# Performance work log

Hardware: AMD Instinct MI355X
Metric: run time of the kernel (lower is better)

The kernel has to match this reference:

```python
import jax, jax.numpy as jnp
import numpy as np

B, T = 8192, 26
V, E, H, L = 23, 100, 128, 64  # vocab, emb dim, GRU hidden, latent; LSTM hidden = E


def setup_inputs() -> dict:
    key = jax.random.key(0)
    ks = jax.random.split(key, 16)
    rn = lambda k, shape, scale=0.1: (jax.random.normal(k, shape, jnp.float32) * scale)
    emb = rn(ks[0], (V, E)).at[0].set(0.0)  # padding_idx=0 row zeroed
    return {
        "z": jax.random.normal(ks[1], (B, L), jnp.float32),
        "x_in": jax.random.randint(ks[2], (B, T), 0, V),
        "emb": emb,
        "fc_z_w": rn(ks[3], (H, L)), "fc_z_b": rn(ks[4], (H,)),
        "gru_wih": rn(ks[5], (3 * H, E)), "gru_whh": rn(ks[6], (3 * H, H)),
        "gru_bih": rn(ks[7], (3 * H,)), "gru_bhh": rn(ks[8], (3 * H,)),
        "lstm_wih": rn(ks[9], (4 * E, H)), "lstm_whh": rn(ks[10], (4 * E, E)),
        "lstm_bih": rn(ks[11], (4 * E,)), "lstm_bhh": rn(ks[12], (4 * E,)),
        "out_w": rn(ks[13], (V, E)), "out_b": rn(ks[14], (V,)),
    }


def _gru(e, h0, Wih, Whh, bih, bhh):
    # e: (B,T,E); precompute input projections for all steps, scan over T.
    xg = jnp.einsum('bti,gi->btg', e, Wih) + bih  # (B,T,3H)

    def step(h, x):
        hg = h @ Whh.T + bhh
        xr, xz, xn = jnp.split(x, 3, axis=-1)
        hr, hz, hn = jnp.split(hg, 3, axis=-1)
        r = jax.nn.sigmoid(xr + hr)
        zg = jax.nn.sigmoid(xz + hz)
        n = jnp.tanh(xn + r * hn)
        h_new = (1.0 - zg) * n + zg * h
        return h_new, h_new

    _, ys = jax.lax.scan(step, h0, jnp.swapaxes(xg, 0, 1))  # (T,B,H)
    return jnp.swapaxes(ys, 0, 1)


def _lstm(x, h0, c0, Wih, Whh, bih, bhh):
    xg = jnp.einsum('bti,gi->btg', x, Wih) + bih  # (B,T,4E)

    def step(hc, xt):
        h, c = hc
        g = xt + h @ Whh.T + bhh
        i, f, gg, o = jnp.split(g, 4, axis=-1)
        c_new = jax.nn.sigmoid(f) * c + jax.nn.sigmoid(i) * jnp.tanh(gg)
        h_new = jax.nn.sigmoid(o) * jnp.tanh(c_new)
        return (h_new, c_new), h_new

    _, ys = jax.lax.scan(step, (h0, c0), jnp.swapaxes(xg, 0, 1))
    return jnp.swapaxes(ys, 0, 1)


def reference(z, x_in, emb, fc_z_w, fc_z_b, gru_wih, gru_whh, gru_bih, gru_bhh,
              lstm_wih, lstm_whh, lstm_bih, lstm_bhh, out_w, out_b):
    h0 = jnp.tanh(z @ fc_z_w.T + fc_z_b)            # (B,H)
    e = emb[x_in]                                    # (B,T,E)
    y = _gru(e, h0, gru_wih, gru_whh, gru_bih, gru_bhh)           # (B,T,H)
    zeros = jnp.zeros((z.shape[0], E), dtype=z.dtype)
    y = _lstm(y, zeros, zeros, lstm_wih, lstm_whh, lstm_bih, lstm_bhh)  # (B,T,E)
    logits = jnp.einsum('bte,ve->btv', y, out_w) + out_b          # (B,T,V)
    return logits
```

## Files before the change

### kernel.cpp

```cpp
#include <hip/hip_runtime.h>
#include <stdint.h>
#include <stddef.h>

#define BB 8192
#define TT 26
#define VV 23
#define EE 100
#define HH 128
#define LL 64

typedef __attribute__((ext_vector_type(8))) short bf16x8;
typedef __attribute__((ext_vector_type(4))) float f32x4;

#define MFMA(a, b, c) __builtin_amdgcn_mfma_f32_16x16x32_bf16((a), (b), (c), 0, 0, 0)

#define OFF_GRUW   0ull
#define OFF_TBL    98304ull
#define OFF_LSTMW  122880ull
#define OFF_OUTW   352256ull
#define OFF_FCZW   360448ull
#define OFF_LBIAS  376832ull

#define L_LW    0
#define L_HF    114688
#define L_LH    122880
#define L_IDX   131072
#define L_TOTAL 131520

__device__ __forceinline__ void force_frag(bf16x8& v) { asm volatile("" : "+v"(v)); }

__device__ __forceinline__ unsigned short f2bf(float f) {
  union { float f; unsigned u; } v; v.f = f;
  unsigned u = v.u;
  return (unsigned short)((u + 0x7FFFu + ((u >> 16) & 1u)) >> 16);
}
__device__ __forceinline__ unsigned short f2bf_fast(float f) {
  union { float f; unsigned u; } v; v.f = f;
  return (unsigned short)((v.u + 0x8000u) >> 16);
}
#define LOG2E 1.4426950408889634f
__device__ __forceinline__ float sigm(float x) {
  return __builtin_amdgcn_rcpf(1.0f + __builtin_amdgcn_exp2f(-x * LOG2E));
}
__device__ __forceinline__ float tanh_(float x) {
  return __builtin_fmaf(-2.0f,
      __builtin_amdgcn_rcpf(1.0f + __builtin_amdgcn_exp2f(x * (2.0f * LOG2E))), 1.0f);
}

__global__ __launch_bounds__(512) void prep_table_kernel(
    const float* __restrict__ emb, const float* __restrict__ gru_wih,
    const float* __restrict__ gru_bih, char* __restrict__ ws)
{
  __shared__ float emb_s[VV * EE];
  __shared__ float wih_s[16 * EE];
  __shared__ float bih_s[16];
  const int tid = threadIdx.x;
  const int ct  = blockIdx.x;
  const int n0  = ct * 16;

  for (int i = tid; i < VV * EE; i += 512) emb_s[i] = emb[i];
  for (int i = tid; i < 16 * EE; i += 512) wih_s[i] = gru_wih[n0 * EE + i];
  if (tid < 16) bih_s[tid] = gru_bih[n0 + tid];
  __syncthreads();

  const int j    = tid & 7;
  const int lane = (tid >> 3) & 63;
  const int n16  = lane & 15;
  const int k    = ((lane >> 4) & 3) * 8 + j;
  float v = 0.0f;
  if (k < VV) {
    const float* ep = emb_s + k * EE;
    const float* wp = wih_s + n16 * EE;
    float s0 = 0.f, s1 = 0.f, s2 = 0.f, s3 = 0.f;
#pragma unroll 5
    for (int m = 0; m < EE; m += 4) {
      s0 += ep[m] * wp[m];         s1 += ep[m + 1] * wp[m + 1];
      s2 += ep[m + 2] * wp[m + 2]; s3 += ep[m + 3] * wp[m + 3];
    }
    v = bih_s[n16] + ((s0 + s1) + (s2 + s3));
  }
  *(unsigned short*)(ws + OFF_TBL + (size_t)(ct * 512 + tid) * 2) = f2bf(v);
}

__global__ __launch_bounds__(256) void prep_main_kernel(
    const float* __restrict__ fc_z_w, const float* __restrict__ gru_whh,
    const float* __restrict__ lstm_wih, const float* __restrict__ lstm_whh,
    const float* __restrict__ lstm_bih, const float* __restrict__ lstm_bhh,
    const float* __restrict__ out_w, char* __restrict__ ws)
{
  int e = blockIdx.x * 256 + threadIdx.x;

  if (e < 49152) {
    int j = e & 7, lane = (e >> 3) & 63, kc = (e >> 9) & 3, ct = e >> 11;
    int n = ct * 16 + (lane & 15);
    int k = kc * 32 + ((lane >> 4) & 3) * 8 + j;
    *(unsigned short*)(ws + OFF_GRUW + (size_t)e * 2) = f2bf(gru_whh[n * HH + k]);
    return;
  }
  e -= 49152;
  if (e < 114688) {
    int j = e & 7, lane = (e >> 3) & 63, kc = (e >> 9) & 7, ct = e >> 12;
    int row = ct * 16 + (lane & 15);
    int g = row / 112, c = row % 112;
    int q = (lane >> 4) & 3;
    float v = 0.0f;
    if (c < EE) {
      if (kc < 4) {
        int k = kc * 32 + q * 8 + j;
        v = lstm_wih[(g * EE + c) * HH + k];
      } else {
        int k = (kc - 4) * 32 + q * 8 + j;
        if (k < EE) v = lstm_whh[(g * EE + c) * EE + k];
      }
    }
    *(unsigned short*)(ws + OFF_LSTMW + (size_t)e * 2) = f2bf(v);
    return;
  }
  e -= 114688;
  if (e < 4096) {
    int j = e & 7, lane = (e >> 3) & 63, kc = (e >> 9) & 3, ct = e >> 11;
    int n = ct * 16 + (lane & 15);
    int k = kc * 32 + ((lane >> 4) & 3) * 8 + j;
    float v = (n < VV && k < EE) ? out_w[n * EE + k] : 0.0f;
    *(unsigned short*)(ws + OFF_OUTW + (size_t)e * 2) = f2bf(v);
    return;
  }
  e -= 4096;
  if (e < 8192) {
    int j = e & 7, lane = (e >> 3) & 63, kc = (e >> 9) & 1, ct = e >> 10;
    int n = ct * 16 + (lane & 15);
    int k = kc * 32 + ((lane >> 4) & 3) * 8 + j;
    *(unsigned short*)(ws + OFF_FCZW + (size_t)e * 2) = f2bf(fc_z_w[n * LL + k]);
    return;
  }
  e -= 8192;
  if (e < 448) {
    int g = e / 112, c = e % 112;
    float v = (c < EE) ? (lstm_bih[g * EE + c] + lstm_bhh[g * EE + c]) : 0.0f;
    *(float*)(ws + OFF_LBIAS + (size_t)e * 4) = v;
  }
}

__global__ __launch_bounds__(1024, 4) void fused_kernel(
    const float* __restrict__ z, const int* __restrict__ x_in,
    const float* __restrict__ fc_z_b, const float* __restrict__ gru_bhh,
    const unsigned short* __restrict__ gruw, const unsigned short* __restrict__ tbl,
    const unsigned short* __restrict__ fczw,
    const unsigned short* __restrict__ lstmw, const float* __restrict__ lbias,
    const float* __restrict__ out_b, const unsigned short* __restrict__ outw,
    float* __restrict__ out)
{
  extern __shared__ char smem[];
  unsigned short* lwlds = (unsigned short*)(smem + L_LW);
  char*           hfrag = smem + L_HF;
  char*           lhbuf = smem + L_LH;
  unsigned char*  idx_lds = (unsigned char*)(smem + L_IDX);

  const int tid  = threadIdx.x;
  const int wv   = tid >> 6;
  const int lane = tid & 63;
  const int l15  = lane & 15;
  const int q    = (lane >> 4) & 3;
  const int blk  = blockIdx.x;

  for (int i = tid; i < 4096; i += 1024)
    ((unsigned short*)lhbuf)[i] = 0;
  for (int f = tid; f < 7168; f += 1024) {
    int frag_i = f >> 6, within = f & 63;
    int ct = frag_i >> 2, kcl = frag_i & 3;
    *(bf16x8*)((char*)lwlds + (size_t)frag_i * 1024 + within * 16) =
        *(const bf16x8*)(lstmw + ((size_t)(ct * 8 + 4 + kcl)) * 512 + within * 8);
  }

  if (wv < 8) {
    {
      int rid = wv * 64 + lane;
      for (int i = rid; i < TT * 16; i += 512) {
        int t = i >> 4, r = i & 15;
        idx_lds[i] = (unsigned char)x_in[(blk * 16 + r) * TT + t];
      }
    }
    bf16x8 gw[3][4], tw[3];
#pragma unroll
    for (int g = 0; g < 3; g++) {
      int ct = g * 8 + wv;
#pragma unroll
      for (int kc = 0; kc < 4; kc++) {
        gw[g][kc] = *(const bf16x8*)(gruw + (size_t)(ct * 4 + kc) * 512 + lane * 8);
        force_frag(gw[g][kc]);
      }
      tw[g] = *(const bf16x8*)(tbl + (size_t)ct * 512 + lane * 8);
      force_frag(tw[g]);
    }
    const int col = wv * 16 + l15;
    const float b_r = gru_bhh[0 * HH + col];
    const float b_z = gru_bhh[1 * HH + col];
    const float b_n = gru_bhh[2 * HH + col];
    const int wbase = (col >> 5) * 512 + ((col >> 3) & 3) * 128 + (col & 7);

    float h[4];
    {
      bf16x8 fw0 = *(const bf16x8*)(fczw + (size_t)(wv * 2 + 0) * 512 + lane * 8);
      bf16x8 fw1 = *(const bf16x8*)(fczw + (size_t)(wv * 2 + 1) * 512 + lane * 8);
      const float* zp = z + (size_t)(blk * 16 + l15) * LL + q * 8;
      f32x4 z0 = *(const f32x4*)(zp);
      f32x4 z1 = *(const f32x4*)(zp + 4);
      f32x4 z2 = *(const f32x4*)(zp + 32);
      f32x4 z3 = *(const f32x4*)(zp + 36);
      bf16x8 za0, za1;
#pragma unroll
      for (int j = 0; j < 4; j++) {
        za0[j]     = (short)f2bf(z0[j]);
        za0[4 + j] = (short)f2bf(z1[j]);
        za1[j]     = (short)f2bf(z2[j]);
        za1[4 + j] = (short)f2bf(z3[j]);
      }
      float fzb = fc_z_b[col];
      f32x4 acc = {fzb, fzb, fzb, fzb};
      acc = MFMA(za0, fw0, acc);
      acc = MFMA(za1, fw1, acc);
#pragma unroll
      for (int i = 0; i < 4; i++) {
        h[i] = tanh_(acc[i]);
        ((unsigned short*)hfrag)[wbase + (q * 4 + i) * 8] = f2bf_fast(h[i]);
      }
    }
    __syncthreads();

    for (int p = 0; p < TT + 2; p++) {
      if (p < TT) {
        int iv = idx_lds[p * 16 + l15];
        bf16x8 oh;
#pragma unroll
        for (int j = 0; j < 8; j++)
          oh[j] = (short)((iv == q * 8 + j) ? 0x3F80 : 0);

        f32x4 ar  = {b_r, b_r, b_r, b_r};
        f32x4 az  = {b_z, b_z, b_z, b_z};
        f32x4 ahn = {b_n, b_n, b_n, b_n};
        f32x4 axn = {0.0f, 0.0f, 0.0f, 0.0f};
        ar  = MFMA(oh, tw[0], ar);
        az  = MFMA(oh, tw[1], az);
        axn = MFMA(oh, tw[2], axn);

        bf16x8 a[4];
#pragma unroll
        for (int kc = 0; kc < 4; kc++)
          a[kc] = *(const bf16x8*)(hfrag + (p & 1) * 4096 + kc * 1024 + lane * 16);
#pragma unroll
        for (int kc = 0; kc < 4; kc++) {
          ar  = MFMA(a[kc], gw[0][kc], ar);
          az  = MFMA(a[kc], gw[1][kc], az);
          ahn = MFMA(a[kc], gw[2][kc], ahn);
        }
#pragma unroll
        for (int i = 0; i < 4; i++) {
          float r  = sigm(ar[i]);
          float zg = sigm(az[i]);
          float n  = tanh_(__builtin_fmaf(r, ahn[i], axn[i]));
          h[i] = __builtin_fmaf(zg, h[i] - n, n);
          ((unsigned short*)(hfrag + ((p + 1) & 1) * 4096))[wbase + (q * 4 + i) * 8]
              = f2bf_fast(h[i]);
        }
      }
      __syncthreads();
    }
  } else if (wv < 15) {
    const int tile = wv - 8;
    bf16x8 lwy[4][4];
#pragma unroll
    for (int g = 0; g < 4; g++)
#pragma unroll
      for (int kc = 0; kc < 4; kc++) {
        lwy[g][kc] = *(const bf16x8*)(lstmw + (size_t)((g * 7 + tile) * 8 + kc) * 512 + lane * 8);
        force_frag(lwy[g][kc]);
      }
    const int col = tile * 16 + l15;
    float b[4];
#pragma unroll
    for (int g = 0; g < 4; g++) b[g] = lbias[g * 112 + col];
    const int wbase = (col >> 5) * 512 + ((col >> 3) & 3) * 128 + (col & 7);
    float c[4] = {0, 0, 0, 0};
    __syncthreads();

    for (int p = 0; p < TT + 2; p++) {
      if (p >= 1 && p <= TT) {
        f32x4 ai = {b[0], b[0], b[0], b[0]};
        f32x4 af = {b[1], b[1], b[1], b[1]};
        f32x4 ag = {b[2], b[2], b[2], b[2]};
        f32x4 ao = {b[3], b[3], b[3], b[3]};
#pragma unroll
        for (int kc = 0; kc < 4; kc++) {
          bf16x8 ya = *(const bf16x8*)(hfrag + (p & 1) * 4096 + kc * 1024 + lane * 16);
          ai = MFMA(ya, lwy[0][kc], ai);
          af = MFMA(ya, lwy[1][kc], af);
          ag = MFMA(ya, lwy[2][kc], ag);
          ao = MFMA(ya, lwy[3][kc], ao);
        }
#pragma unroll
        for (int kc = 0; kc < 4; kc++) {
          bf16x8 ha = *(const bf16x8*)(lhbuf + ((p - 1) & 1) * 4096 + kc * 1024 + lane * 16);
          const char* wb = (const char*)lwlds + (size_t)(tile * 4 + kc) * 1024 + lane * 16;
          bf16x8 w0 = *(const bf16x8*)(wb);
          bf16x8 w1 = *(const bf16x8*)(wb + 28672);
          bf16x8 w2 = *(const bf16x8*)(wb + 2 * 28672);
          bf16x8 w3 = *(const bf16x8*)(wb + 3 * 28672);
          ai = MFMA(ha, w0, ai);
          af = MFMA(ha, w1, af);
          ag = MFMA(ha, w2, ag);
          ao = MFMA(ha, w3, ao);
        }
#pragma unroll
        for (int i = 0; i < 4; i++) {
          float ii = sigm(ai[i]), ff = sigm(af[i]);
          float gg = tanh_(ag[i]), oo = sigm(ao[i]);
          float cn = __builtin_fmaf(ff, c[i], ii * gg);
          c[i] = cn;
          ((unsigned short*)(lhbuf + (p & 1) * 4096))[wbase + (q * 4 + i) * 8]
              = f2bf_fast(oo * tanh_(cn));
        }
      }
      __syncthreads();
    }
  } else {
    bf16x8 ow[2][4];
#pragma unroll
    for (int ct = 0; ct < 2; ct++)
#pragma unroll
      for (int kc = 0; kc < 4; kc++) {
        ow[ct][kc] = *(const bf16x8*)(outw + (size_t)(ct * 4 + kc) * 512 + lane * 8);
        force_frag(ow[ct][kc]);
      }
    float ob[2];
#pragma unroll
    for (int ct = 0; ct < 2; ct++) {
      int cv = ct * 16 + l15;
      ob[ct] = (cv < VV) ? out_b[cv] : 0.0f;
    }
    __syncthreads();

    for (int p = 0; p < TT + 2; p++) {
      if (p >= 2) {
        const int t = p - 2;
        bf16x8 ha[4];
#pragma unroll
        for (int kc = 0; kc < 4; kc++)
          ha[kc] = *(const bf16x8*)(lhbuf + ((p - 1) & 1) * 4096 + kc * 1024 + lane * 16);
#pragma unroll
        for (int ct = 0; ct < 2; ct++) {
          f32x4 acc = {ob[ct], ob[ct], ob[ct], ob[ct]};
#pragma unroll
          for (int kc = 0; kc < 4; kc++)
            acc = MFMA(ha[kc], ow[ct][kc], acc);
          int cv = ct * 16 + l15;
          if (cv < VV) {
#pragma unroll
            for (int i = 0; i < 4; i++) {
              int rowg = blk * 16 + q * 4 + i;
              out[((size_t)rowg * TT + t) * VV + cv] = acc[i];
            }
          }
        }
      }
      __syncthreads();
    }
  }
}

extern "C" void kernel_launch(void* const* d_in, const int* in_sizes, int n_in,
                              void* d_out, int out_size, void* d_ws, size_t ws_size,
                              hipStream_t stream) {
  (void)in_sizes; (void)n_in; (void)out_size; (void)ws_size;
  const float* z        = (const float*)d_in[0];
  const int*   x_in     = (const int*)  d_in[1];
  const float* emb      = (const float*)d_in[2];
  const float* fc_z_w   = (const float*)d_in[3];
  const float* fc_z_b   = (const float*)d_in[4];
  const float* gru_wih  = (const float*)d_in[5];
  const float* gru_whh  = (const float*)d_in[6];
  const float* gru_bih  = (const float*)d_in[7];
  const float* gru_bhh  = (const float*)d_in[8];
  const float* lstm_wih = (const float*)d_in[9];
  const float* lstm_whh = (const float*)d_in[10];
  const float* lstm_bih = (const float*)d_in[11];
  const float* lstm_bhh = (const float*)d_in[12];
  const float* out_w    = (const float*)d_in[13];
  const float* out_b    = (const float*)d_in[14];
  char*  ws  = (char*)d_ws;
  float* out = (float*)d_out;

  const unsigned short* gruw  = (const unsigned short*)(ws + OFF_GRUW);
  const unsigned short* tblp  = (const unsigned short*)(ws + OFF_TBL);
  const unsigned short* lstmw = (const unsigned short*)(ws + OFF_LSTMW);
  const unsigned short* outw  = (const unsigned short*)(ws + OFF_OUTW);
  const unsigned short* fczw  = (const unsigned short*)(ws + OFF_FCZW);
  const float*          lbias = (const float*)(ws + OFF_LBIAS);

  static int lds_attr_set = 0;
  (void)lds_attr_set;
  hipFuncSetAttribute((const void*)fused_kernel,
                      hipFuncAttributeMaxDynamicSharedMemorySize, L_TOTAL);

  prep_main_kernel<<<690, 256, 0, stream>>>(fc_z_w, gru_whh, lstm_wih, lstm_whh,
                                            lstm_bih, lstm_bhh, out_w, ws);
  prep_table_kernel<<<24, 512, 0, stream>>>(emb, gru_wih, gru_bih, ws);
  fused_kernel<<<512, 1024, L_TOTAL, stream>>>(z, x_in, fc_z_b, gru_bhh,
                                               gruw, tblp, fczw, lstmw, lbias,
                                               out_b, outw, out);
}
```

Before: 185.7 us.

## Process 32 rows per block and fold weight prep into fused kernel

Each block now handles two 16-row batch sub-tiles (32 rows), halving the grid to 256 blocks. Each block therefore loads its register and LDS weights once and reuses them for twice the rows, and each per-timestep barrier is shared across both sub-tiles. The separate prep_main kernel is removed; weights are read as fp32 and converted to bf16 fragments inside the fused kernel. The trade-off is fewer blocks, hence less parallelism across CUs (256 blocks, fewer than one per CU if 1024-thread blocks can run several per CU), and more LDS per block.

```diff
diff --git a/kernel.cpp b/kernel.cpp
--- a/kernel.cpp
+++ b/kernel.cpp
@@ -14,18 +14,13 @@
 
 #define MFMA(a, b, c) __builtin_amdgcn_mfma_f32_16x16x32_bf16((a), (b), (c), 0, 0, 0)
 
-#define OFF_GRUW   0ull
-#define OFF_TBL    98304ull
-#define OFF_LSTMW  122880ull
-#define OFF_OUTW   352256ull
-#define OFF_FCZW   360448ull
-#define OFF_LBIAS  376832ull
+#define OFF_TBL 0ull
 
 #define L_LW    0
 #define L_HF    114688
-#define L_LH    122880
-#define L_IDX   131072
-#define L_TOTAL 131520
+#define L_LH    131072
+#define L_IDX   147456
+#define L_TOTAL 148288
 
 __device__ __forceinline__ void force_frag(bf16x8& v) { asm volatile("" : "+v"(v)); }
 
@@ -45,6 +40,15 @@
 __device__ __forceinline__ float tanh_(float x) {
   return __builtin_fmaf(-2.0f,
       __builtin_amdgcn_rcpf(1.0f + __builtin_amdgcn_exp2f(x * (2.0f * LOG2E))), 1.0f);
+}
+
+__device__ __forceinline__ bf16x8 ldfrag8(const float* __restrict__ p) {
+  f32x4 a = *(const f32x4*)(p);
+  f32x4 b = *(const f32x4*)(p + 4);
+  bf16x8 r;
+#pragma unroll
+  for (int j = 0; j < 4; j++) { r[j] = (short)f2bf(a[j]); r[4 + j] = (short)f2bf(b[j]); }
+  return r;
 }
 
 __global__ __launch_bounds__(512) void prep_table_kernel(
@@ -82,78 +86,19 @@
   *(unsigned short*)(ws + OFF_TBL + (size_t)(ct * 512 + tid) * 2) = f2bf(v);
 }
 
-__global__ __launch_bounds__(256) void prep_main_kernel(
-    const float* __restrict__ fc_z_w, const float* __restrict__ gru_whh,
-    const float* __restrict__ lstm_wih, const float* __restrict__ lstm_whh,
-    const float* __restrict__ lstm_bih, const float* __restrict__ lstm_bhh,
-    const float* __restrict__ out_w, char* __restrict__ ws)
-{
-  int e = blockIdx.x * 256 + threadIdx.x;
-
-  if (e < 49152) {
-    int j = e & 7, lane = (e >> 3) & 63, kc = (e >> 9) & 3, ct = e >> 11;
-    int n = ct * 16 + (lane & 15);
-    int k = kc * 32 + ((lane >> 4) & 3) * 8 + j;
-    *(unsigned short*)(ws + OFF_GRUW + (size_t)e * 2) = f2bf(gru_whh[n * HH + k]);
-    return;
-  }
-  e -= 49152;
-  if (e < 114688) {
-    int j = e & 7, lane = (e >> 3) & 63, kc = (e >> 9) & 7, ct = e >> 12;
-    int row = ct * 16 + (lane & 15);
-    int g = row / 112, c = row % 112;
-    int q = (lane >> 4) & 3;
-    float v = 0.0f;
-    if (c < EE) {
-      if (kc < 4) {
-        int k = kc * 32 + q * 8 + j;
-        v = lstm_wih[(g * EE + c) * HH + k];
-      } else {
-        int k = (kc - 4) * 32 + q * 8 + j;
-        if (k < EE) v = lstm_whh[(g * EE + c) * EE + k];
-      }
-    }
-    *(unsigned short*)(ws + OFF_LSTMW + (size_t)e * 2) = f2bf(v);
-    return;
-  }
-  e -= 114688;
-  if (e < 4096) {
-    int j = e & 7, lane = (e >> 3) & 63, kc = (e >> 9) & 3, ct = e >> 11;
-    int n = ct * 16 + (lane & 15);
-    int k = kc * 32 + ((lane >> 4) & 3) * 8 + j;
-    float v = (n < VV && k < EE) ? out_w[n * EE + k] : 0.0f;
-    *(unsigned short*)(ws + OFF_OUTW + (size_t)e * 2) = f2bf(v);
-    return;
-  }
-  e -= 4096;
-  if (e < 8192) {
-    int j = e & 7, lane = (e >> 3) & 63, kc = (e >> 9) & 1, ct = e >> 10;
-    int n = ct * 16 + (lane & 15);
-    int k = kc * 32 + ((lane >> 4) & 3) * 8 + j;
-    *(unsigned short*)(ws + OFF_FCZW + (size_t)e * 2) = f2bf(fc_z_w[n * LL + k]);
-    return;
-  }
-  e -= 8192;
-  if (e < 448) {
-    int g = e / 112, c = e % 112;
-    float v = (c < EE) ? (lstm_bih[g * EE + c] + lstm_bhh[g * EE + c]) : 0.0f;
-    *(float*)(ws + OFF_LBIAS + (size_t)e * 4) = v;
-  }
-}
-
 __global__ __launch_bounds__(1024, 4) void fused_kernel(
     const float* __restrict__ z, const int* __restrict__ x_in,
     const float* __restrict__ fc_z_b, const float* __restrict__ gru_bhh,
-    const unsigned short* __restrict__ gruw, const unsigned short* __restrict__ tbl,
-    const unsigned short* __restrict__ fczw,
-    const unsigned short* __restrict__ lstmw, const float* __restrict__ lbias,
-    const float* __restrict__ out_b, const unsigned short* __restrict__ outw,
-    float* __restrict__ out)
+    const float* __restrict__ gru_whh, const float* __restrict__ fc_z_w,
+    const float* __restrict__ lstm_wih, const float* __restrict__ lstm_whh,
+    const float* __restrict__ lstm_bih, const float* __restrict__ lstm_bhh,
+    const float* __restrict__ out_w, const float* __restrict__ out_b,
+    const unsigned short* __restrict__ tbl, float* __restrict__ out)
 {
   extern __shared__ char smem[];
-  unsigned short* lwlds = (unsigned short*)(smem + L_LW);
-  char*           hfrag = smem + L_HF;
-  char*           lhbuf = smem + L_LH;
+  char*           lwlds   = smem + L_LW;
+  char*           hfrag   = smem + L_HF;
+  char*           lhbuf   = smem + L_LH;
   unsigned char*  idx_lds = (unsigned char*)(smem + L_IDX);
 
   const int tid  = threadIdx.x;
@@ -163,161 +108,183 @@
   const int q    = (lane >> 4) & 3;
   const int blk  = blockIdx.x;
 
-  for (int i = tid; i < 4096; i += 1024)
+  for (int i = tid; i < 8192; i += 1024)
     ((unsigned short*)lhbuf)[i] = 0;
   for (int f = tid; f < 7168; f += 1024) {
     int frag_i = f >> 6, within = f & 63;
     int ct = frag_i >> 2, kcl = frag_i & 3;
-    *(bf16x8*)((char*)lwlds + (size_t)frag_i * 1024 + within * 16) =
-        *(const bf16x8*)(lstmw + ((size_t)(ct * 8 + 4 + kcl)) * 512 + within * 8);
+    int row = ct * 16 + (within & 15);
+    int g = row / 112, c = row - g * 112;
+    int k0 = kcl * 32 + ((within >> 4) & 3) * 8;
+    bf16x8 vv;
+#pragma unroll
+    for (int j = 0; j < 8; j++) {
+      int k = k0 + j;
+      float v = (c < EE && k < EE) ? lstm_whh[(g * EE + c) * EE + k] : 0.0f;
+      vv[j] = (short)f2bf(v);
+    }
+    *(bf16x8*)(lwlds + (size_t)frag_i * 1024 + within * 16) = vv;
   }
 
   if (wv < 8) {
     {
       int rid = wv * 64 + lane;
-      for (int i = rid; i < TT * 16; i += 512) {
-        int t = i >> 4, r = i & 15;
-        idx_lds[i] = (unsigned char)x_in[(blk * 16 + r) * TT + t];
-      }
-    }
+      for (int i = rid; i < TT * 32; i += 512) {
+        int t = i >> 5, r = i & 31;
+        idx_lds[i] = (unsigned char)x_in[(blk * 32 + r) * TT + t];
+      }
+    }
+    const int col = wv * 16 + l15;
     bf16x8 gw[3][4], tw[3];
 #pragma unroll
     for (int g = 0; g < 3; g++) {
-      int ct = g * 8 + wv;
+      int n = (g * 8 + wv) * 16 + l15;
 #pragma unroll
       for (int kc = 0; kc < 4; kc++) {
-        gw[g][kc] = *(const bf16x8*)(gruw + (size_t)(ct * 4 + kc) * 512 + lane * 8);
+        gw[g][kc] = ldfrag8(gru_whh + (size_t)n * HH + kc * 32 + q * 8);
         force_frag(gw[g][kc]);
       }
-      tw[g] = *(const bf16x8*)(tbl + (size_t)ct * 512 + lane * 8);
+      tw[g] = *(const bf16x8*)(tbl + (size_t)(g * 8 + wv) * 512 + lane * 8);
       force_frag(tw[g]);
     }
-    const int col = wv * 16 + l15;
     const float b_r = gru_bhh[0 * HH + col];
     const float b_z = gru_bhh[1 * HH + col];
     const float b_n = gru_bhh[2 * HH + col];
     const int wbase = (col >> 5) * 512 + ((col >> 3) & 3) * 128 + (col & 7);
 
-    float h[4];
+    float h[2][4];
     {
-      bf16x8 fw0 = *(const bf16x8*)(fczw + (size_t)(wv * 2 + 0) * 512 + lane * 8);
-      bf16x8 fw1 = *(const bf16x8*)(fczw + (size_t)(wv * 2 + 1) * 512 + lane * 8);
-      const float* zp = z + (size_t)(blk * 16 + l15) * LL + q * 8;
-      f32x4 z0 = *(const f32x4*)(zp);
-      f32x4 z1 = *(const f32x4*)(zp + 4);
-      f32x4 z2 = *(const f32x4*)(zp + 32);
-      f32x4 z3 = *(const f32x4*)(zp + 36);
-      bf16x8 za0, za1;
-#pragma unroll
-      for (int j = 0; j < 4; j++) {
-        za0[j]     = (short)f2bf(z0[j]);
-        za0[4 + j] = (short)f2bf(z1[j]);
-        za1[j]     = (short)f2bf(z2[j]);
-        za1[4 + j] = (short)f2bf(z3[j]);
-      }
+      bf16x8 fw0 = ldfrag8(fc_z_w + (size_t)col * LL + 0 * 32 + q * 8);
+      bf16x8 fw1 = ldfrag8(fc_z_w + (size_t)col * LL + 1 * 32 + q * 8);
       float fzb = fc_z_b[col];
-      f32x4 acc = {fzb, fzb, fzb, fzb};
-      acc = MFMA(za0, fw0, acc);
-      acc = MFMA(za1, fw1, acc);
-#pragma unroll
-      for (int i = 0; i < 4; i++) {
-        h[i] = tanh_(acc[i]);
-        ((unsigned short*)hfrag)[wbase + (q * 4 + i) * 8] = f2bf_fast(h[i]);
+#pragma unroll
+      for (int s = 0; s < 2; s++) {
+        const float* zp = z + (size_t)(blk * 32 + s * 16 + l15) * LL + q * 8;
+        f32x4 z0 = *(const f32x4*)(zp);
+        f32x4 z1 = *(const f32x4*)(zp + 4);
+        f32x4 z2 = *(const f32x4*)(zp + 32);
+        f32x4 z3 = *(const f32x4*)(zp + 36);
+        bf16x8 za0, za1;
+#pragma unroll
+        for (int j = 0; j < 4; j++) {
+          za0[j]     = (short)f2bf(z0[j]);
+          za0[4 + j] = (short)f2bf(z1[j]);
+          za1[j]     = (short)f2bf(z2[j]);
+          za1[4 + j] = (short)f2bf(z3[j]);
+        }
+        f32x4 acc = {fzb, fzb, fzb, fzb};
+        acc = MFMA(za0, fw0, acc);
+        acc = MFMA(za1, fw1, acc);
+#pragma unroll
+        for (int i = 0; i < 4; i++) {
+          h[s][i] = tanh_(acc[i]);
+          ((unsigned short*)(hfrag + s * 4096))[wbase + (q * 4 + i) * 8] = f2bf_fast(h[s][i]);
+        }
       }
     }
     __syncthreads();
 
     for (int p = 0; p < TT + 2; p++) {
       if (p < TT) {
-        int iv = idx_lds[p * 16 + l15];
-        bf16x8 oh;
-#pragma unroll
-        for (int j = 0; j < 8; j++)
-          oh[j] = (short)((iv == q * 8 + j) ? 0x3F80 : 0);
-
-        f32x4 ar  = {b_r, b_r, b_r, b_r};
-        f32x4 az  = {b_z, b_z, b_z, b_z};
-        f32x4 ahn = {b_n, b_n, b_n, b_n};
-        f32x4 axn = {0.0f, 0.0f, 0.0f, 0.0f};
-        ar  = MFMA(oh, tw[0], ar);
-        az  = MFMA(oh, tw[1], az);
-        axn = MFMA(oh, tw[2], axn);
-
-        bf16x8 a[4];
-#pragma unroll
-        for (int kc = 0; kc < 4; kc++)
-          a[kc] = *(const bf16x8*)(hfrag + (p & 1) * 4096 + kc * 1024 + lane * 16);
-#pragma unroll
-        for (int kc = 0; kc < 4; kc++) {
-          ar  = MFMA(a[kc], gw[0][kc], ar);
-          az  = MFMA(a[kc], gw[1][kc], az);
-          ahn = MFMA(a[kc], gw[2][kc], ahn);
-        }
-#pragma unroll
-        for (int i = 0; i < 4; i++) {
-          float r  = sigm(ar[i]);
-          float zg = sigm(az[i]);
-          float n  = tanh_(__builtin_fmaf(r, ahn[i], axn[i]));
-          h[i] = __builtin_fmaf(zg, h[i] - n, n);
-          ((unsigned short*)(hfrag + ((p + 1) & 1) * 4096))[wbase + (q * 4 + i) * 8]
-              = f2bf_fast(h[i]);
+#pragma unroll
+        for (int s = 0; s < 2; s++) {
+          int iv = idx_lds[p * 32 + s * 16 + l15];
+          bf16x8 oh;
+#pragma unroll
+          for (int j = 0; j < 8; j++)
+            oh[j] = (short)((iv == q * 8 + j) ? 0x3F80 : 0);
+
+          f32x4 ar  = {b_r, b_r, b_r, b_r};
+          f32x4 az  = {b_z, b_z, b_z, b_z};
+          f32x4 ahn = {b_n, b_n, b_n, b_n};
+          f32x4 axn = {0.0f, 0.0f, 0.0f, 0.0f};
+          ar  = MFMA(oh, tw[0], ar);
+          az  = MFMA(oh, tw[1], az);
+          axn = MFMA(oh, tw[2], axn);
+
+          bf16x8 a[4];
+#pragma unroll
+          for (int kc = 0; kc < 4; kc++)
+            a[kc] = *(const bf16x8*)(hfrag + (p & 1) * 8192 + s * 4096 + kc * 1024 + lane * 16);
+#pragma unroll
+          for (int kc = 0; kc < 4; kc++) {
+            ar  = MFMA(a[kc], gw[0][kc], ar);
+            az  = MFMA(a[kc], gw[1][kc], az);
+            ahn = MFMA(a[kc], gw[2][kc], ahn);
+          }
+#pragma unroll
+          for (int i = 0; i < 4; i++) {
+            float r  = sigm(ar[i]);
+            float zg = sigm(az[i]);
+            float n  = tanh_(__builtin_fmaf(r, ahn[i], axn[i]));
+            h[s][i] = __builtin_fmaf(zg, h[s][i] - n, n);
+            ((unsigned short*)(hfrag + ((p + 1) & 1) * 8192 + s * 4096))[wbase + (q * 4 + i) * 8]
+                = f2bf_fast(h[s][i]);
+          }
         }
       }
       __syncthreads();
     }
   } else if (wv < 15) {
     const int tile = wv - 8;
+    const int col  = tile * 16 + l15;
     bf16x8 lwy[4][4];
 #pragma unroll
     for (int g = 0; g < 4; g++)
 #pragma unroll
       for (int kc = 0; kc < 4; kc++) {
-        lwy[g][kc] = *(const bf16x8*)(lstmw + (size_t)((g * 7 + tile) * 8 + kc) * 512 + lane * 8);
+        bf16x8 w;
+        if (col < EE) w = ldfrag8(lstm_wih + (size_t)(g * EE + col) * HH + kc * 32 + q * 8);
+        else { bf16x8 zz = {0,0,0,0,0,0,0,0}; w = zz; }
+        lwy[g][kc] = w;
         force_frag(lwy[g][kc]);
       }
-    const int col = tile * 16 + l15;
     float b[4];
 #pragma unroll
-    for (int g = 0; g < 4; g++) b[g] = lbias[g * 112 + col];
+    for (int g = 0; g < 4; g++)
+      b[g] = (col < EE) ? (lstm_bih[g * EE + col] + lstm_bhh[g * EE + col]) : 0.0f;
     const int wbase = (col >> 5) * 512 + ((col >> 3) & 3) * 128 + (col & 7);
-    float c[4] = {0, 0, 0, 0};
+    float c[2][4] = {{0, 0, 0, 0}, {0, 0, 0, 0}};
     __syncthreads();
 
     for (int p = 0; p < TT + 2; p++) {
       if (p >= 1 && p <= TT) {
-        f32x4 ai = {b[0], b[0], b[0], b[0]};
-        f32x4 af = {b[1], b[1], b[1], b[1]};
-        f32x4 ag = {b[2], b[2], b[2], b[2]};
-        f32x4 ao = {b[3], b[3], b[3], b[3]};
-#pragma unroll
-        for (int kc = 0; kc < 4; kc++) {
-          bf16x8 ya = *(const bf16x8*)(hfrag + (p & 1) * 4096 + kc * 1024 + lane * 16);
-          ai = MFMA(ya, lwy[0][kc], ai);
-          af = MFMA(ya, lwy[1][kc], af);
-          ag = MFMA(ya, lwy[2][kc], ag);
-          ao = MFMA(ya, lwy[3][kc], ao);
-        }
-#pragma unroll
-        for (int kc = 0; kc < 4; kc++) {
-          bf16x8 ha = *(const bf16x8*)(lhbuf + ((p - 1) & 1) * 4096 + kc * 1024 + lane * 16);
-          const char* wb = (const char*)lwlds + (size_t)(tile * 4 + kc) * 1024 + lane * 16;
-          bf16x8 w0 = *(const bf16x8*)(wb);
-          bf16x8 w1 = *(const bf16x8*)(wb + 28672);
-          bf16x8 w2 = *(const bf16x8*)(wb + 2 * 28672);
-          bf16x8 w3 = *(const bf16x8*)(wb + 3 * 28672);
-          ai = MFMA(ha, w0, ai);
-          af = MFMA(ha, w1, af);
-          ag = MFMA(ha, w2, ag);
-          ao = MFMA(ha, w3, ao);
-        }
-#pragma unroll
-        for (int i = 0; i < 4; i++) {
-          float ii = sigm(ai[i]), ff = sigm(af[i]);
-          float gg = tanh_(ag[i]), oo = sigm(ao[i]);
-          float cn = __builtin_fmaf(ff, c[i], ii * gg);
-          c[i] = cn;
-          ((unsigned short*)(lhbuf + (p & 1) * 4096))[wbase + (q * 4 + i) * 8]
-              = f2bf_fast(oo * tanh_(cn));
+#pragma unroll
+        for (int s = 0; s < 2; s++) {
+          f32x4 ai = {b[0], b[0], b[0], b[0]};
+          f32x4 af = {b[1], b[1], b[1], b[1]};
+          f32x4 ag = {b[2], b[2], b[2], b[2]};
+          f32x4 ao = {b[3], b[3], b[3], b[3]};
+#pragma unroll
+          for (int kc = 0; kc < 4; kc++) {
+            bf16x8 ya = *(const bf16x8*)(hfrag + (p & 1) * 8192 + s * 4096 + kc * 1024 + lane * 16);
+            ai = MFMA(ya, lwy[0][kc], ai);
+            af = MFMA(ya, lwy[1][kc], af);
+            ag = MFMA(ya, lwy[2][kc], ag);
+            ao = MFMA(ya, lwy[3][kc], ao);
+          }
+#pragma unroll
+          for (int kc = 0; kc < 4; kc++) {
+            bf16x8 ha = *(const bf16x8*)(lhbuf + ((p - 1) & 1) * 8192 + s * 4096 + kc * 1024 + lane * 16);
+            const char* wb = lwlds + (size_t)(tile * 4 + kc) * 1024 + lane * 16;
+            bf16x8 w0 = *(const bf16x8*)(wb);
+            bf16x8 w1 = *(const bf16x8*)(wb + 28672);
+            bf16x8 w2 = *(const bf16x8*)(wb + 2 * 28672);
+            bf16x8 w3 = *(const bf16x8*)(wb + 3 * 28672);
+            ai = MFMA(ha, w0, ai);
+            af = MFMA(ha, w1, af);
+            ag = MFMA(ha, w2, ag);
+            ao = MFMA(ha, w3, ao);
+          }
+#pragma unroll
+          for (int i = 0; i < 4; i++) {
+            float ii = sigm(ai[i]), ff = sigm(af[i]);
+            float gg = tanh_(ag[i]), oo = sigm(ao[i]);
+            float cn = __builtin_fmaf(ff, c[s][i], ii * gg);
+            c[s][i] = cn;
+            ((unsigned short*)(lhbuf + (p & 1) * 8192 + s * 4096))[wbase + (q * 4 + i) * 8]
+                = f2bf_fast(oo * tanh_(cn));
+          }
         }
       }
       __syncthreads();
@@ -325,12 +292,25 @@
   } else {
     bf16x8 ow[2][4];
 #pragma unroll
-    for (int ct = 0; ct < 2; ct++)
+    for (int ct = 0; ct < 2; ct++) {
+      int n = ct * 16 + l15;
 #pragma unroll
       for (int kc = 0; kc < 4; kc++) {
-        ow[ct][kc] = *(const bf16x8*)(outw + (size_t)(ct * 4 + kc) * 512 + lane * 8);
+        bf16x8 w;
+        if (n < VV && kc < 3) {
+          w = ldfrag8(out_w + (size_t)n * EE + kc * 32 + q * 8);
+        } else {
+#pragma unroll
+          for (int j = 0; j < 8; j++) {
+            int k = kc * 32 + q * 8 + j;
+            float v = (n < VV && k < EE) ? out_w[(size_t)n * EE + k] : 0.0f;
+            w[j] = (short)f2bf(v);
+          }
+        }
+        ow[ct][kc] = w;
         force_frag(ow[ct][kc]);
       }
+    }
     float ob[2];
 #pragma unroll
     for (int ct = 0; ct < 2; ct++) {
@@ -342,22 +322,25 @@
     for (int p = 0; p < TT + 2; p++) {
       if (p >= 2) {
         const int t = p - 2;
-        bf16x8 ha[4];
-#pragma unroll
-        for (int kc = 0; kc < 4; kc++)
-          ha[kc] = *(const bf16x8*)(lhbuf + ((p - 1) & 1) * 4096 + kc * 1024 + lane * 16);
-#pragma unroll
-        for (int ct = 0; ct < 2; ct++) {
-          f32x4 acc = {ob[ct], ob[ct], ob[ct], ob[ct]};
+#pragma unroll
+        for (int s = 0; s < 2; s++) {
+          bf16x8 ha[4];
 #pragma unroll
           for (int kc = 0; kc < 4; kc++)
-            acc = MFMA(ha[kc], ow[ct][kc], acc);
-          int cv = ct * 16 + l15;
-          if (cv < VV) {
-#pragma unroll
-            for (int i = 0; i < 4; i++) {
-              int rowg = blk * 16 + q * 4 + i;
-              out[((size_t)rowg * TT + t) * VV + cv] = acc[i];
+            ha[kc] = *(const bf16x8*)(lhbuf + ((p - 1) & 1) * 8192 + s * 4096 + kc * 1024 + lane * 16);
+#pragma unroll
+          for (int ct = 0; ct < 2; ct++) {
+            f32x4 acc = {ob[ct], ob[ct], ob[ct], ob[ct]};
+#pragma unroll
+            for (int kc = 0; kc < 4; kc++)
+              acc = MFMA(ha[kc], ow[ct][kc], acc);
+            int cv = ct * 16 + l15;
+            if (cv < VV) {
+#pragma unroll
+              for (int i = 0; i < 4; i++) {
+                int rowg = blk * 32 + s * 16 + q * 4 + i;
+                out[((size_t)rowg * TT + t) * VV + cv] = acc[i];
+              }
             }
           }
         }
@@ -389,22 +372,15 @@
   char*  ws  = (char*)d_ws;
   float* out = (float*)d_out;
 
-  const unsigned short* gruw  = (const unsigned short*)(ws + OFF_GRUW);
-  const unsigned short* tblp  = (const unsigned short*)(ws + OFF_TBL);
-  const unsigned short* lstmw = (const unsigned short*)(ws + OFF_LSTMW);
-  const unsigned short* outw  = (const unsigned short*)(ws + OFF_OUTW);
-  const unsigned short* fczw  = (const unsigned short*)(ws + OFF_FCZW);
-  const float*          lbias = (const float*)(ws + OFF_LBIAS);
-
-  static int lds_attr_set = 0;
-  (void)lds_attr_set;
+  const unsigned short* tblp = (const unsigned short*)(ws + OFF_TBL);
+
   hipFuncSetAttribute((const void*)fused_kernel,
                       hipFuncAttributeMaxDynamicSharedMemorySize, L_TOTAL);
 
-  prep_main_kernel<<<690, 256, 0, stream>>>(fc_z_w, gru_whh, lstm_wih, lstm_whh,
-                                            lstm_bih, lstm_bhh, out_w, ws);
   prep_table_kernel<<<24, 512, 0, stream>>>(emb, gru_wih, gru_bih, ws);
-  fused_kernel<<<512, 1024, L_TOTAL, stream>>>(z, x_in, fc_z_b, gru_bhh,
-                                               gruw, tblp, fczw, lstmw, lbias,
-                                               out_b, outw, out);
-}
+  fused_kernel<<<256, 1024, L_TOTAL, stream>>>(z, x_in, fc_z_b, gru_bhh,
+                                               gru_whh, fc_z_w,
+                                               lstm_wih, lstm_whh,
+                                               lstm_bih, lstm_bhh,
+                                               out_w, out_b, tblp, out);
+}
```

Measured after the change: 207.8 us. 11.9% more time.
